# Optimization experiments

Hardware: AMD Instinct MI355X
Metric: run time of the kernel (lower is better)

The kernel has to match this reference:

```python
import jax, jax.numpy as jnp
import numpy as np

C = 256   # d_model
L = 2     # num_decoder_layers
B = 4
H = 128
W = 128
WH = 8    # dec_win_h
WW = 16   # dec_win_w
EPS = 1e-5


def _gn(x, w, b):
    # GroupNorm with 1 group: normalize over (C,H,W) per sample, per-channel affine
    mu = jnp.mean(x, axis=(1, 2, 3), keepdims=True)
    var = jnp.mean((x - mu) ** 2, axis=(1, 2, 3), keepdims=True)
    xn = (x - mu) * jax.lax.rsqrt(var + EPS)
    return xn * w[:, None, None] + b[:, None, None]


def _conv1x1(x, w, b):
    # x: [B,C,H,W], w: [O,C], b: [O]
    return jnp.einsum('bchw,oc->bohw', x, w) + b[:, None, None]


def _avgpool3(x):
    # AvgPool2d(3, stride=1, padding=1, count_include_pad=False)
    dims = (1, 1, 3, 3)
    strides = (1, 1, 1, 1)
    pad = [(0, 0), (0, 0), (1, 1), (1, 1)]
    s = jax.lax.reduce_window(x, 0.0, jax.lax.add, dims, strides, pad)
    ones = jnp.ones((1, 1) + x.shape[2:], x.dtype)
    cnt = jax.lax.reduce_window(ones, 0.0, jax.lax.add, dims, strides, pad)
    return s / cnt


def _mix(x):
    # PoolFormer token mixer: avgpool(x) - x
    return _avgpool3(x) - x


def _win_part(x, wh, ww):
    # [B,C,H,W] -> [B*nWin, C, wh, ww]
    b, c, h, w = x.shape
    x = x.reshape(b, c, h // wh, wh, w // ww, ww)
    x = x.transpose(0, 2, 4, 1, 3, 5)
    return x.reshape(-1, c, wh, ww)


def _agp(tgt, mem, qw, qb, kw, kb, vw, vb):
    # AttentionGuidedPooling; NOTE: torch uses .view(B,-1,C) on [B,C,H,W],
    # a raw reshape (not a transpose) -- replicated faithfully here.
    bw, c, h, w = mem.shape
    n = h * w
    q = _conv1x1(tgt, qw, qb).reshape(bw, n, c)
    k = _conv1x1(mem, kw, kb).reshape(bw, n, c)
    v = _conv1x1(mem, vw, vb).reshape(bw, n, c)
    attn = jax.nn.softmax(jnp.einsum('bnc,bmc->bnm', q, k), axis=-1)
    out = jnp.einsum('bnm,bmc->bnc', attn, v)
    return out.reshape(bw, c, h, w)


def _layer(tgt, mem, p):
    (gn1_w, gn1_b, gn2_w, gn2_b, ls1, ls2, ls3,
     qw, qb, kw, kb, vw, vb, fc1_w, fc1_b, fc2_w, fc2_b) = p
    tgt2 = tgt + ls1[:, None, None] * _mix(_gn(tgt, gn1_w, gn1_b))
    guided = _agp(tgt, mem, qw, qb, kw, kb, vw, vb)
    tgt3 = tgt2 + guided
    tgt3 = tgt2 + ls2[:, None, None] * _mix(_gn(tgt3, gn1_w, gn1_b))
    h = _gn(tgt3, gn2_w, gn2_b)
    h = _conv1x1(h, fc1_w, fc1_b)
    h = jax.nn.gelu(h, approximate=False)  # torch nn.GELU default (erf)
    h = _conv1x1(h, fc2_w, fc2_b)
    return tgt3 + ls3[:, None, None] * h


def setup_inputs() -> dict:
    key = jax.random.key(0)
    ks = jax.random.split(key, 16)
    s = 0.02
    inp = {
        'src': jax.random.normal(ks[0], (B, C, H, W), jnp.float32),
        'query_feats': jax.random.normal(ks[1], (B, C, H, W), jnp.float32),
        'gn1_w': jnp.ones((L, C), jnp.float32),
        'gn1_b': jnp.zeros((L, C), jnp.float32),
        'gn2_w': jnp.ones((L, C), jnp.float32),
        'gn2_b': jnp.zeros((L, C), jnp.float32),
        'ls1': 1e-5 * jnp.ones((L, C), jnp.float32),
        'ls2': 1e-5 * jnp.ones((L, C), jnp.float32),
        'ls3': 1e-5 * jnp.ones((L, C), jnp.float32),
        'qw': s * jax.random.normal(ks[2], (L, C, C), jnp.float32),
        'qb': jnp.zeros((L, C), jnp.float32),
        'kw': s * jax.random.normal(ks[3], (L, C, C), jnp.float32),
        'kb': jnp.zeros((L, C), jnp.float32),
        'vw': s * jax.random.normal(ks[4], (L, C, C), jnp.float32),
        'vb': jnp.zeros((L, C), jnp.float32),
        'fc1_w': s * jax.random.normal(ks[5], (L, 2 * C, C), jnp.float32),
        'fc1_b': jnp.zeros((L, 2 * C), jnp.float32),
        'fc2_w': s * jax.random.normal(ks[6], (L, C, 2 * C), jnp.float32),
        'fc2_b': jnp.zeros((L, C), jnp.float32),
        'gnf_w': jnp.ones((C,), jnp.float32),
        'gnf_b': jnp.zeros((C,), jnp.float32),
    }
    return inp


def reference(src, query_feats, gn1_w, gn1_b, gn2_w, gn2_b, ls1, ls2, ls3,
              qw, qb, kw, kb, vw, vb, fc1_w, fc1_b, fc2_w, fc2_b, gnf_w, gnf_b):
    # pq_stride=8 -> div_ratio=1: memory windows same size as tgt windows
    mem = _win_part(src, WH, WW)
    out = _win_part(query_feats, WH, WW)
    for l in range(L):
        p = (gn1_w[l], gn1_b[l], gn2_w[l], gn2_b[l], ls1[l], ls2[l], ls3[l],
             qw[l], qb[l], kw[l], kb[l], vw[l], vb[l],
             fc1_w[l], fc1_b[l], fc2_w[l], fc2_b[l])
        out = _layer(out, mem, p)
    out = _gn(out, gnf_w, gnf_b)
    # window reverse -> [B, C, H, W] -> sequence [B, H*W, C]
    nwh, nww = H // WH, W // WW
    x = out.reshape(B, nwh, nww, C, WH, WW).transpose(0, 3, 1, 4, 2, 5)
    x = x.reshape(B, C, H * W)
    hs = jnp.swapaxes(x, 1, 2)[None]        # [1, B, N, C]
    return jnp.swapaxes(hs, 1, 2)           # [1, N, B, C]
```

## Files before the change

kernel.cpp:

```cpp
#include <hip/hip_runtime.h>
#include <hip/hip_bf16.h>

typedef __hip_bfloat16 bf16_t;
typedef short bf16x8 __attribute__((ext_vector_type(8)));
typedef float f32x4 __attribute__((ext_vector_type(4)));

__device__ __forceinline__ float bfr(unsigned short u) {
  return __uint_as_float(((unsigned int)u) << 16);
}
__device__ __forceinline__ float b2f(bf16_t h) { return __bfloat162float(h); }
__device__ __forceinline__ bf16_t f2b(float f) { return __float2bfloat16(f); }
__device__ __forceinline__ unsigned short f2bu(float f) {
  union { bf16_t h; unsigned short u; } cv; cv.h = __float2bfloat16(f); return cv.u;
}
__device__ __forceinline__ void unpk2(unsigned int u, float& a, float& b) {
  a = __uint_as_float(u << 16);
  b = __uint_as_float(u & 0xffff0000u);
}
__device__ __forceinline__ void ld8b(const bf16_t* p, float* o) {
  uint4 v = *(const uint4*)p;
  unpk2(v.x,o[0],o[1]); unpk2(v.y,o[2],o[3]); unpk2(v.z,o[4],o[5]); unpk2(v.w,o[6],o[7]);
}
__device__ __forceinline__ void unpk8(uint4 v, float* o) {
  unpk2(v.x,o[0],o[1]); unpk2(v.y,o[2],o[3]); unpk2(v.z,o[4],o[5]); unpk2(v.w,o[6],o[7]);
}
__device__ __forceinline__ int flag_of(const void* w) {
  return (*(const unsigned int*)w == 0x3F803F80u) ? 0 : 1;
}

typedef __attribute__((address_space(3))) void lds_t;
typedef __attribute__((address_space(1))) void glb_t;
__device__ __forceinline__ void gll16(const void* g, void* l) {
  __builtin_amdgcn_global_load_lds((glb_t*)g, (lds_t*)l, 16, 0, 0);
}

struct Srcs { const void* p[18]; };

__global__ __launch_bounds__(256)
void k_cvtall(Srcs a, bf16_t* __restrict__ PR) {
  const int ck = blockIdx.x*256 + threadIdx.x;
  if (ck >= 115520) return;
  constexpr int N8[18]  = {64,64,64,64,64,64,64,64,64,128,64,32,32,16384,16384,16384,32768,32768};
  constexpr int DOF[18] = {0,512,1024,1536,2048,2560,3072,3584,4096,4608,5632,6144,6400,8192,139264,270336,401408,663552};
  int s = 0, base = 0, doff = 0, cum = 0;
#pragma unroll
  for (int i = 0; i < 17; ++i) {
    cum += N8[i];
    if (ck >= cum) { s = i + 1; base = cum; doff = DOF[i + 1]; }
  }
  const int o8 = ck - base;
  const void* sp = a.p[s];
  const int fl = flag_of(a.p[0]);
  uint4 w;
  if (fl) {
    const float4* f = (const float4*)sp;
    float4 v0 = f[o8*2], v1 = f[o8*2+1];
    w.x = ((unsigned)f2bu(v0.y)<<16) | f2bu(v0.x);
    w.y = ((unsigned)f2bu(v0.w)<<16) | f2bu(v0.z);
    w.z = ((unsigned)f2bu(v1.y)<<16) | f2bu(v1.x);
    w.w = ((unsigned)f2bu(v1.w)<<16) | f2bu(v1.z);
  } else {
    w = ((const uint4*)sp)[o8];
  }
  *(uint4*)(PR + doff + o8*8) = w;
}

__global__ __launch_bounds__(256)
void k_xt2(const void* __restrict__ inA, bf16_t* __restrict__ outA,
           const void* __restrict__ inB, bf16_t* __restrict__ outB,
           const void* __restrict__ flagw) {
  __shared__ unsigned short L[128*130];
  const void* in = blockIdx.z ? inB : inA;
  bf16_t* out = blockIdx.z ? outB : outA;
  const int win = blockIdx.x, tile = blockIdx.y, tid = threadIdx.x;
  const int IC = tile << 7;
  const int fl = flag_of(flagw);
  const int b = win >> 7, whi = (win >> 3) & 15, wwi = win & 7;

  for (int i = 0; i < 8; ++i) {
    int idx = tid + (i<<8);
    int r = idx >> 4, ch = idx & 15;
    unsigned int w0, w1, w2, w3;
    int c = IC + r;
    int hq = ch >> 1, wq = (ch & 1) << 3;
    long gaddr = ((long)((b<<8) + c) << 14) + ((whi<<3) + hq)*128 + (wwi<<4) + wq;
    if (fl) {
      const float* gp = (const float*)in + gaddr;
      float4 aa = *(const float4*)gp, bb = *(const float4*)(gp+4);
      w0 = ((unsigned)f2bu(aa.y)<<16)|f2bu(aa.x); w1 = ((unsigned)f2bu(aa.w)<<16)|f2bu(aa.z);
      w2 = ((unsigned)f2bu(bb.y)<<16)|f2bu(bb.x); w3 = ((unsigned)f2bu(bb.w)<<16)|f2bu(bb.z);
    } else {
      uint4 v = *(const uint4*)((const bf16_t*)in + gaddr);
      w0 = v.x; w1 = v.y; w2 = v.z; w3 = v.w;
    }
    unsigned int* Lp = (unsigned int*)L;
    int u32o = (r*130 + (ch<<3)) >> 1;
    Lp[u32o+0] = w0; Lp[u32o+1] = w1; Lp[u32o+2] = w2; Lp[u32o+3] = w3;
  }
  __syncthreads();
  for (int i = 0; i < 8; ++i) {
    int idx = tid + (i<<8);
    int q = idx >> 4, ch = idx & 15;
    unsigned short pk[8];
#pragma unroll
    for (int j = 0; j < 8; ++j) pk[j] = L[((ch<<3) + j)*130 + q];
    *(uint4*)(out + (long)win*32768 + (long)q*256 + IC + (ch<<3)) = *(uint4*)pk;
  }
}

__global__ __launch_bounds__(256) void k_statsP(const bf16_t* __restrict__ X, float* __restrict__ st) {
  __shared__ float s1[256], s2[256];
  int w = blockIdx.x, tid = threadIdx.x;
  const bf16_t* x = X + ((long)w << 15);
  float a = 0.f, b = 0.f;
  for (int i = tid*8; i < 32768; i += 2048) {
    float t[8]; ld8b(x + i, t);
#pragma unroll
    for (int j = 0; j < 8; ++j) { a += t[j]; b += t[j]*t[j]; }
  }
  s1[tid] = a; s2[tid] = b;
  __syncthreads();
  for (int off = 128; off > 0; off >>= 1) {
    if (tid < off) { s1[tid] += s1[tid+off]; s2[tid] += s2[tid+off]; }
    __syncthreads();
  }
  if (tid == 0) {
    float mu = s1[0] * (1.0f/32768.0f);
    float var = s2[0] * (1.0f/32768.0f) - mu*mu;
    st[(w<<1)]   = mu;
    st[(w<<1)+1] = rsqrtf(var + 1e-5f);
  }
}

template<int GATH, int GN2>
__global__ __launch_bounds__(256)
void k_poolf(const bf16_t* __restrict__ Xp, const bf16_t* __restrict__ Gc,
             bf16_t* __restrict__ Out,
             const bf16_t* __restrict__ lsv, const bf16_t* __restrict__ gw,
             bf16_t* __restrict__ G2,
             const bf16_t* __restrict__ g2w, const bf16_t* __restrict__ g2b) {
  __shared__ unsigned short L[32768];
  __shared__ float s1[256], s2[256];
  __shared__ float mr[2];
  const int win = blockIdx.x;
  const int tid = threadIdx.x;
  const long wb = (long)win << 15;
  float a = 0.f, b = 0.f;

#pragma unroll 4
  for (int i = 0; i < 16; ++i) {
    int k = (i<<8) + tid;
    int p = k >> 5, c8 = k & 31;
    uint4 v = *(const uint4*)(Xp + wb + (p<<8) + (c8<<3));
    *(uint4*)&L[(p<<8) + ((c8 ^ (p & 31))<<3)] = v;
    if (!GATH) {
      float t[8]; unpk8(v, t);
#pragma unroll
      for (int j = 0; j < 8; ++j) { a += t[j]; b += t[j]*t[j]; }
    }
  }
  if (GATH) {
    __syncthreads();
#pragma unroll 4
    for (int i = 0; i < 16; ++i) {
      int k = (i<<8) + tid;
      int c = k >> 4, p0 = (k & 15) << 3;
      uint4 gv = *(const uint4*)(Gc + wb + (c<<7) + p0);
      float g[8]; unpk8(gv, g);
      int ch = c >> 3, cl = c & 7;
#pragma unroll
      for (int j = 0; j < 8; ++j) {
        int p = p0 + j;
        int idx = (p<<8) + ((ch ^ (p & 31))<<3) + cl;
        float xx = bfr(L[idx]) + g[j];
        a += xx; b += xx*xx;
        L[idx] = f2bu(xx);
      }
    }
  }
  s1[tid] = a; s2[tid] = b;
  __syncthreads();
  for (int off = 128; off > 0; off >>= 1) {
    if (tid < off) { s1[tid] += s1[tid+off]; s2[tid] += s2[tid+off]; }
    __syncthreads();
  }
  if (tid == 0) {
    float mu = s1[0] * (1.0f/32768.0f);
    float var = s2[0] * (1.0f/32768.0f) - mu*mu;
    mr[0] = mu; mr[1] = rsqrtf(var + 1e-5f);
  }
  __syncthreads();
  const float rstd = mr[1];
  const int c = tid;
  const int ch = c >> 3, cl = c & 7;
  const float scl = b2f(lsv[c]) * b2f(gw[c]) * rstd;
  float oa = 0.f, ob = 0.f;

  float rm1[16], r0[16], rp1[16];
#pragma unroll
  for (int ww = 0; ww < 16; ++ww) {
    int p = ww;
    r0[ww] = bfr(L[(p<<8) + ((ch ^ (p & 31))<<3) + cl]);
    int p1 = 16 + ww;
    rp1[ww] = bfr(L[(p1<<8) + ((ch ^ (p1 & 31))<<3) + cl]);
  }
  for (int h = 0; h < 8; ++h) {
    float cs[16];
    float hc = 1.f + (h > 0 ? 1.f : 0.f) + (h < 7 ? 1.f : 0.f);
#pragma unroll
    for (int ww = 0; ww < 16; ++ww)
      cs[ww] = r0[ww] + (h > 0 ? rm1[ww] : 0.f) + (h < 7 ? rp1[ww] : 0.f);
#pragma unroll
    for (int ww = 0; ww < 16; ++ww) {
      float s = cs[ww];
      float wc = 1.f;
      if (ww > 0)  { s += cs[ww-1]; wc += 1.f; }
      if (ww < 15) { s += cs[ww+1]; wc += 1.f; }
      float avg = s / (hc * wc);
      float xx = r0[ww];
      int p = (h<<4) + ww;
      float base = xx;
      if (GATH) base = bfr(*(const unsigned short*)(Xp + wb + (p<<8) + c));
      float val = base + scl * (avg - xx);
      if (GN2) {
        oa += val; ob += val*val;
        L[(p<<8) + ((ch ^ (p & 31))<<3) + cl] = f2bu(val);
      }
      Out[wb + (p<<8) + c] = f2b(val);
    }
#pragma unroll
    for (int ww = 0; ww < 16; ++ww) { rm1[ww] = r0[ww]; r0[ww] = rp1[ww]; }
    if (h < 6) {
      int hp = (h+2) << 4;
#pragma unroll
      for (int ww = 0; ww < 16; ++ww) {
        int p = hp + ww;
        rp1[ww] = bfr(L[(p<<8) + ((ch ^ (p & 31))<<3) + cl]);
      }
    }
  }
  if (GN2) {
    __syncthreads();
    s1[tid] = oa; s2[tid] = ob;
    __syncthreads();
    for (int off = 128; off > 0; off >>= 1) {
      if (tid < off) { s1[tid] += s1[tid+off]; s2[tid] += s2[tid+off]; }
      __syncthreads();
    }
    if (tid == 0) {
      float mu = s1[0] * (1.0f/32768.0f);
      float var = s2[0] * (1.0f/32768.0f) - mu*mu;
      mr[0] = mu; mr[1] = rsqrtf(var + 1e-5f);
    }
    __syncthreads();
    const float mu2 = mr[0], rs2 = mr[1];
#pragma unroll 4
    for (int i = 0; i < 16; ++i) {
      int k = (i<<8) + tid;
      int p = k >> 5, cv = k & 31;
      uint4 v = *(const uint4*)&L[(p<<8) + ((cv ^ (p & 31))<<3)];
      float t[8]; unpk8(v, t);
      uint4 wv = *(const uint4*)(g2w + (cv<<3));
      uint4 bv = *(const uint4*)(g2b + (cv<<3));
      float wf[8], bf2[8]; unpk8(wv, wf); unpk8(bv, bf2);
      unsigned short pk[8];
#pragma unroll
      for (int j = 0; j < 8; ++j) pk[j] = f2bu((t[j]-mu2)*rs2*wf[j] + bf2[j]);
      *(uint4*)(G2 + wb + (p<<8) + (cv<<3)) = *(uint4*)pk;
    }
  }
}

#define GM_QKV  0
#define GM_NM   1
#define GM_GELU 2
#define GM_RES  3

template<int MODE>
__global__ __launch_bounds__(256, 2)
void k_gemm(const bf16_t* __restrict__ A, long sA, int lda,
            const bf16_t* __restrict__ B0, const bf16_t* __restrict__ B1,
            long sB, int ldb,
            bf16_t* __restrict__ Y, long sY, int ldy,
            const bf16_t* __restrict__ bias,
            const bf16_t* __restrict__ res, long sR,
            const bf16_t* __restrict__ ls,
            int K) {
  __shared__ uint4 LB[2048];
  unsigned short* As = (unsigned short*)LB;
  unsigned short* Bs = (unsigned short*)LB + 8192;
  unsigned short* E  = (unsigned short*)LB;
  const int win = blockIdx.x;
  const int tid = threadIdx.x;
  const int w = tid >> 6, lane = tid & 63;
  const int l15 = lane & 15, quad = lane >> 4;
  const int m0w = (w >> 1) << 6, n0w = (w & 1) << 6;

  int sel = 0, m0;
  const bf16_t *Ab, *Bb; bf16_t* Yb; const bf16_t* biasb = nullptr;
  if (MODE == GM_QKV) {
    sel = blockIdx.y >> 1; m0 = (blockIdx.y & 1) << 7;
    Ab = A + sel*131072 + (long)m0*lda;
    Bb = (sel ? B1 : B0) + (long)win*sB;
    Yb = Y + (long)sel*16777216 + (long)win*sY;
    biasb = bias + sel*512 + m0;
  } else {
    m0 = blockIdx.y << 7;
    Ab = A + (long)win*sA + (long)m0*lda;
    Bb = B0 + (long)win*sB;
    Yb = Y + (long)win*sY;
    if (bias) biasb = bias + m0;
  }
  const bool CT = (MODE == GM_QKV) && (sel < 2);

  int rr_[4], co_[4], lo_[4];
#pragma unroll
  for (int j = 0; j < 4; ++j) {
    int ck = (j<<8) + (w<<6) + lane;
    int r = ck >> 3;
    rr_[j] = r;
    co_[j] = ((ck & 7) ^ (r & 7)) << 3;
    lo_[j] = ((j<<8) + (w<<6)) << 3;
  }

  f32x4 acc[4][4];
#pragma unroll
  for (int i = 0; i < 4; ++i)
#pragma unroll
    for (int j = 0; j < 4; ++j) acc[i][j] = (f32x4){0.f,0.f,0.f,0.f};

  for (int k0 = 0; k0 < K; k0 += 64) {
#pragma unroll
    for (int j = 0; j < 4; ++j) {
      gll16(Ab + (long)rr_[j]*lda + k0 + co_[j], As + lo_[j]);
      gll16(Bb + (long)rr_[j]*ldb + k0 + co_[j], Bs + lo_[j]);
    }
    __syncthreads();
#pragma unroll
    for (int kk = 0; kk < 2; ++kk) {
      bf16x8 af[4], bv[4];
#pragma unroll
      for (int im = 0; im < 4; ++im) {
        int R = m0w + (im<<4) + l15;
        af[im] = *(const bf16x8*)&As[(R<<6) + ((((kk<<2)+quad) ^ (R&7))<<3)];
      }
#pragma unroll
      for (int in = 0; in < 4; ++in) {
        int R = n0w + (in<<4) + l15;
        bv[in] = *(const bf16x8*)&Bs[(R<<6) + ((((kk<<2)+quad) ^ (R&7))<<3)];
      }
      if (CT) {
#pragma unroll
        for (int im = 0; im < 4; ++im)
#pragma unroll
          for (int in = 0; in < 4; ++in)
            acc[im][in] = __builtin_amdgcn_mfma_f32_16x16x32_bf16(bv[in], af[im], acc[im][in], 0, 0, 0);
      } else {
#pragma unroll
        for (int im = 0; im < 4; ++im)
#pragma unroll
          for (int in = 0; in < 4; ++in)
            acc[im][in] = __builtin_amdgcn_mfma_f32_16x16x32_bf16(af[im], bv[in], acc[im][in], 0, 0, 0);
      }
    }
    __syncthreads();
  }

  if (MODE == GM_QKV && sel == 2) {
#pragma unroll
    for (int im = 0; im < 4; ++im) {
#pragma unroll
      for (int in = 0; in < 4; ++in) {
        f32x4 v = acc[im][in];
        int tok = n0w + (in<<4) + l15;
        int c0 = m0w + (im<<4) + (quad<<2);
        int u0 = c0 >> 1;
        float x0 = v[0] + b2f(biasb[c0]);
        float x1 = v[1] + b2f(biasb[c0+1]);
        float x2 = v[2] + b2f(biasb[c0+2]);
        float x3 = v[3] + b2f(biasb[c0+3]);
        int sl = (((u0>>3) ^ (tok&7))<<3) + (u0&7);
        *(unsigned int*)&E[(tok<<6) + sl]       = (unsigned)f2bu(x0) | ((unsigned)f2bu(x2)<<16);
        *(unsigned int*)&E[((128+tok)<<6) + sl] = (unsigned)f2bu(x1) | ((unsigned)f2bu(x3)<<16);
      }
    }
    __syncthreads();
#pragma unroll
    for (int i = 0; i < 8; ++i) {
      int ck = (i<<8) + tid;
      int cp = ck >> 3, u8 = ck & 7;
      uint4 v = *(const uint4*)&E[(cp<<6) + ((u8 ^ (cp&7))<<3)];
      *(uint4*)(Yb + (long)cp*128 + (m0>>1) + (u8<<3)) = v;
    }
    return;
  }

  if (CT) {
#pragma unroll
    for (int half = 0; half < 2; ++half) {
      if (m0w == (half<<6)) {
#pragma unroll
        for (int im = 0; im < 4; ++im) {
          int row = (im<<4) + l15;
          float bm = b2f(biasb[(half<<6) + row]);
#pragma unroll
          for (int in = 0; in < 4; ++in) {
            f32x4 v = acc[im][in];
            unsigned short pk[4];
#pragma unroll
            for (int r = 0; r < 4; ++r) pk[r] = f2bu(v[r] + bm);
            *(ushort4*)&E[row*136 + n0w + (in<<4) + (quad<<2)] = *(ushort4*)pk;
          }
        }
      }
      __syncthreads();
#pragma unroll
      for (int i = 0; i < 4; ++i) {
        int ck = (i<<8) + tid;
        int row = ck >> 4, c8 = (ck & 15) << 3;
        uint4 v = *(const uint4*)&E[row*136 + c8];
        *(uint4*)(Yb + (long)(m0 + (half<<6) + row)*ldy + c8) = v;
      }
      __syncthreads();
    }
    return;
  }

#pragma unroll
  for (int half = 0; half < 2; ++half) {
    if (n0w == (half<<6)) {
#pragma unroll
      for (int in = 0; in < 4; ++in) {
        int row = (in<<4) + l15;
#pragma unroll
        for (int im = 0; im < 4; ++im) {
          f32x4 v = acc[im][in];
          int mb = m0w + (im<<4) + (quad<<2);
          unsigned short pk[4];
#pragma unroll
          for (int r = 0; r < 4; ++r) {
            float x = v[r];
            if (MODE == GM_GELU || MODE == GM_RES) x += b2f(biasb[mb + r]);
            if (MODE == GM_GELU) x = 0.5f * x * (1.0f + erff(x * 0.70710678118654752f));
            pk[r] = f2bu(x);
          }
          *(ushort4*)&E[row*136 + mb] = *(ushort4*)pk;
        }
      }
    }
    __syncthreads();
#pragma unroll
    for (int i = 0; i < 4; ++i) {
      int ck = (i<<8) + tid;
      int rloc = ck >> 4, c8 = (ck & 15) << 3;
      long oadr = (long)((half<<6) + rloc)*ldy + m0 + c8;
      uint4 v = *(const uint4*)&E[rloc*136 + c8];
      if (MODE == GM_RES) {
        float t[8]; unpk8(v, t);
        uint4 rv = *(const uint4*)(res + (long)win*sR + oadr);
        float rf[8]; unpk8(rv, rf);
        uint4 lv = *(const uint4*)(ls + m0 + c8);
        float lf[8]; unpk8(lv, lf);
        unsigned short pk[8];
#pragma unroll
        for (int j = 0; j < 8; ++j) pk[j] = f2bu(rf[j] + lf[j]*t[j]);
        *(uint4*)(Yb + oadr) = *(uint4*)pk;
      } else {
        *(uint4*)(Yb + oadr) = v;
      }
    }
    __syncthreads();
  }
}

__global__ __launch_bounds__(256, 2)
void k_scores(const bf16_t* __restrict__ Kc, const bf16_t* __restrict__ Qc,
              bf16_t* __restrict__ P) {
  __shared__ uint4 LB[2048];
  __shared__ float red[2][2][128];
  unsigned short* As = (unsigned short*)LB;
  unsigned short* Bs = (unsigned short*)LB + 8192;
  const int win = blockIdx.x;
  const int tid = threadIdx.x;
  const int w = tid >> 6, lane = tid & 63;
  const int l15 = lane & 15, quad = lane >> 4;
  const int m0w = (w >> 1) << 6, n0w = (w & 1) << 6;
  const int wrow = w >> 1;
  const bf16_t* Ab = Kc + ((long)win << 15);
  const bf16_t* Bb = Qc + ((long)win << 15);

  int rr_[4], co_[4], lo_[4];
#pragma unroll
  for (int j = 0; j < 4; ++j) {
    int ck = (j<<8) + (w<<6) + lane;
    int r = ck >> 3;
    rr_[j] = r;
    co_[j] = ((ck & 7) ^ (r & 7)) << 3;
    lo_[j] = ((j<<8) + (w<<6)) << 3;
  }

  f32x4 acc[4][4];
#pragma unroll
  for (int i = 0; i < 4; ++i)
#pragma unroll
    for (int j = 0; j < 4; ++j) acc[i][j] = (f32x4){0.f,0.f,0.f,0.f};

  for (int k0 = 0; k0 < 256; k0 += 64) {
#pragma unroll
    for (int j = 0; j < 4; ++j) {
      gll16(Ab + (long)rr_[j]*256 + k0 + co_[j], As + lo_[j]);
      gll16(Bb + (long)rr_[j]*256 + k0 + co_[j], Bs + lo_[j]);
    }
    __syncthreads();
#pragma unroll
    for (int kk = 0; kk < 2; ++kk) {
      bf16x8 af[4], bv[4];
#pragma unroll
      for (int im = 0; im < 4; ++im) {
        int R = m0w + (im<<4) + l15;
        af[im] = *(const bf16x8*)&As[(R<<6) + ((((kk<<2)+quad) ^ (R&7))<<3)];
      }
#pragma unroll
      for (int in = 0; in < 4; ++in) {
        int R = n0w + (in<<4) + l15;
        bv[in] = *(const bf16x8*)&Bs[(R<<6) + ((((kk<<2)+quad) ^ (R&7))<<3)];
      }
#pragma unroll
      for (int im = 0; im < 4; ++im)
#pragma unroll
        for (int in = 0; in < 4; ++in)
          acc[im][in] = __builtin_amdgcn_mfma_f32_16x16x32_bf16(af[im], bv[in], acc[im][in], 0, 0, 0);
    }
    __syncthreads();
  }

  float mx[4];
#pragma unroll
  for (int in = 0; in < 4; ++in) {
    float m = -3.4e38f;
#pragma unroll
    for (int im = 0; im < 4; ++im)
#pragma unroll
      for (int r = 0; r < 4; ++r) m = fmaxf(m, acc[im][in][r]);
    m = fmaxf(m, __shfl_xor(m, 16));
    m = fmaxf(m, __shfl_xor(m, 32));
    mx[in] = m;
  }
  if (quad == 0) {
#pragma unroll
    for (int in = 0; in < 4; ++in) red[0][wrow][n0w + (in<<4) + l15] = mx[in];
  }
  __syncthreads();
  float fm[4];
#pragma unroll
  for (int in = 0; in < 4; ++in) {
    int t = n0w + (in<<4) + l15;
    fm[in] = fmaxf(red[0][0][t], red[0][1][t]);
  }
  float sm[4];
#pragma unroll
  for (int in = 0; in < 4; ++in) {
    float s = 0.f;
#pragma unroll
    for (int im = 0; im < 4; ++im)
#pragma unroll
      for (int r = 0; r < 4; ++r) {
        float e = __expf(acc[im][in][r] - fm[in]);
        acc[im][in][r] = e;
        s += e;
      }
    s += __shfl_xor(s, 16);
    s += __shfl_xor(s, 32);
    sm[in] = s;
  }
  if (quad == 0) {
#pragma unroll
    for (int in = 0; in < 4; ++in) red[1][wrow][n0w + (in<<4) + l15] = sm[in];
  }
  __syncthreads();
  bf16_t* Pw = P + ((long)win << 14);
#pragma unroll
  for (int in = 0; in < 4; ++in) {
    int t = n0w + (in<<4) + l15;
    float inv = 1.0f / (red[1][0][t] + red[1][1][t]);
#pragma unroll
    for (int im = 0; im < 4; ++im) {
      int u = m0w + (im<<4) + (quad<<2);
      unsigned short pk[4];
#pragma unroll
      for (int r = 0; r < 4; ++r) pk[r] = f2bu(acc[im][in][r] * inv);
      *(ushort4*)(Pw + t*128 + u) = *(ushort4*)pk;
    }
  }
}

__global__ void k_final(const bf16_t* __restrict__ Tp, const float* __restrict__ st,
                        const bf16_t* __restrict__ gw, const bf16_t* __restrict__ gb,
                        void* __restrict__ out, const void* __restrict__ flagw) {
  const int fl = flag_of(flagw);
  int idx = blockIdx.x*256 + threadIdx.x;
  int c = idx & 255, p = (idx >> 8) & 127, win = idx >> 15;
  float mu = st[win*2], rs = st[win*2+1];
  float v = (b2f(Tp[idx]) - mu) * rs * b2f(gw[c]) + b2f(gb[c]);
  int b = win >> 7, whi = (win >> 3) & 15, wwi = win & 7;
  int n = ((whi<<3) + (p>>4)) * 128 + (wwi<<4) + (p & 15);
  long o = ((long)((n<<2) + b) << 8) + c;
  if (fl) ((float*)out)[o] = v;
  else    ((bf16_t*)out)[o] = f2b(v);
}

extern "C" void kernel_launch(void* const* d_in, const int* in_sizes, int n_in,
                              void* d_out, int out_size, void* d_ws, size_t ws_size,
                              hipStream_t stream) {
  (void)in_sizes; (void)n_in; (void)out_size; (void)ws_size;
  const void* src   = d_in[0];
  const void* qfeat = d_in[1];

  bf16_t* W    = (bf16_t*)d_ws;
  bf16_t* Tp   = W;
  bf16_t* T2p  = W + 16777216;
  bf16_t* Sp   = W + 33554432;
  bf16_t* slA  = W + 50331648;
  bf16_t* KcGc = W + 67108864;
  bf16_t* Vc   = W + 83886080;
  bf16_t* Hp   = KcGc;
  bf16_t* P    = W + 100663296;
  bf16_t* PR   = W + 109051904;
  float*  ST   = (float*)(W + 110100480);
  float*  st0  = ST;

  bf16_t* gn1w = PR;
  bf16_t* gn2w = PR + 512;
  bf16_t* gn2b = PR + 1024;
  bf16_t* ls1  = PR + 1536;
  bf16_t* ls2  = PR + 2048;
  bf16_t* ls3  = PR + 2560;
  bf16_t* qb   = PR + 3072;
  bf16_t* f1b  = PR + 4608;
  bf16_t* f2bp = PR + 5632;
  bf16_t* gfw  = PR + 6144;
  bf16_t* gfb  = PR + 6400;
  bf16_t* qw   = PR + 8192;
  bf16_t* f1w  = PR + 401408;
  bf16_t* f2w  = PR + 663552;

  Srcs sa;
  const int map[18] = {2,4,5,6,7,8,10,12,14,16,18,19,20,9,11,13,15,17};
  for (int i = 0; i < 18; ++i) sa.p[i] = d_in[map[i]];
  k_cvtall<<<452, 256, 0, stream>>>(sa, PR);

  k_xt2<<<dim3(512,2,2), 256, 0, stream>>>(qfeat, Tp, src, Sp, d_in[2]);

  for (int l = 0; l < 2; ++l) {
    k_poolf<0,0><<<512, 256, 0, stream>>>(Tp, nullptr, T2p, ls1 + l*256, gn1w + l*256,
                                          nullptr, nullptr, nullptr);
    k_gemm<GM_QKV><<<dim3(512,6), 256, 0, stream>>>(
        qw + l*65536, 0, 256, Tp, Sp, 32768, 256, slA, 32768, 128,
        qb + l*256, nullptr, 0, nullptr, 256);
    k_scores<<<512, 256, 0, stream>>>(KcGc, slA, P);
    k_gemm<GM_NM><<<dim3(512,2), 256, 0, stream>>>(
        Vc, 32768, 128, P, nullptr, 16384, 128, KcGc, 32768, 256,
        nullptr, nullptr, 0, nullptr, 128);
    k_poolf<1,1><<<512, 256, 0, stream>>>(T2p, KcGc, Tp, ls2 + l*256, gn1w + l*256,
                                          slA, gn2w + l*256, gn2b + l*256);
    k_gemm<GM_GELU><<<dim3(512,4), 256, 0, stream>>>(
        f1w + l*131072, 0, 256, slA, nullptr, 32768, 256, Hp, 65536, 512,
        f1b + l*512, nullptr, 0, nullptr, 256);
    k_gemm<GM_RES><<<dim3(512,2), 256, 0, stream>>>(
        f2w + l*131072, 0, 512, Hp, nullptr, 65536, 512, Tp, 32768, 256,
        f2bp + l*256, Tp, 32768, ls3 + l*256, 512);
  }

  k_statsP<<<512, 256, 0, stream>>>(Tp, st0);
  k_final<<<65536, 256, 0, stream>>>(Tp, st0, gfw, gfb, d_out, d_in[2]);
}
```

Before: 817.0 us.

## Split poolformer rows across 512 threads, use shuffle reductions, vectorize final GroupNorm

k_poolf now runs 512 threads per window. Each half of the block handles four of the eight window rows, and the LDS swizzle is changed to match. Block reductions use wavefront xor-shuffles plus an 8-entry shared array instead of a 256-step tree with many barriers. The GN2 pass re-reads its values from the global output rather than rewriting them into LDS, since the two halves would otherwise race. The final normalize/scatter kernel now processes 8 channels per thread with vector loads and stores, replacing one element per thread, which cuts its launch to an eighth as many blocks.

```diff
diff --git a/kernel.cpp b/kernel.cpp
--- a/kernel.cpp
+++ b/kernel.cpp
@@ -133,26 +133,26 @@
 }
 
 template<int GATH, int GN2>
-__global__ __launch_bounds__(256)
+__global__ __launch_bounds__(512, 4)
 void k_poolf(const bf16_t* __restrict__ Xp, const bf16_t* __restrict__ Gc,
              bf16_t* __restrict__ Out,
              const bf16_t* __restrict__ lsv, const bf16_t* __restrict__ gw,
              bf16_t* __restrict__ G2,
              const bf16_t* __restrict__ g2w, const bf16_t* __restrict__ g2b) {
   __shared__ unsigned short L[32768];
-  __shared__ float s1[256], s2[256];
+  __shared__ float s1[8], s2[8];
   __shared__ float mr[2];
   const int win = blockIdx.x;
   const int tid = threadIdx.x;
   const long wb = (long)win << 15;
   float a = 0.f, b = 0.f;
 
-#pragma unroll 4
-  for (int i = 0; i < 16; ++i) {
-    int k = (i<<8) + tid;
+#pragma unroll
+  for (int i = 0; i < 8; ++i) {
+    int k = (i<<9) + tid;
     int p = k >> 5, c8 = k & 31;
     uint4 v = *(const uint4*)(Xp + wb + (p<<8) + (c8<<3));
-    *(uint4*)&L[(p<<8) + ((c8 ^ (p & 31))<<3)] = v;
+    *(uint4*)&L[(p<<8) + ((c8 ^ ((p>>3)&7))<<3)] = v;
     if (!GATH) {
       float t[8]; unpk8(v, t);
 #pragma unroll
@@ -161,37 +161,39 @@
   }
   if (GATH) {
     __syncthreads();
-#pragma unroll 4
-    for (int i = 0; i < 16; ++i) {
-      int k = (i<<8) + tid;
+#pragma unroll
+    for (int i = 0; i < 8; ++i) {
+      int k = (i<<9) + tid;
       int c = k >> 4, p0 = (k & 15) << 3;
       uint4 gv = *(const uint4*)(Gc + wb + (c<<7) + p0);
       float g[8]; unpk8(gv, g);
       int ch = c >> 3, cl = c & 7;
+      int sl = ((ch ^ ((p0>>3) & 7))<<3) + cl;
 #pragma unroll
       for (int j = 0; j < 8; ++j) {
-        int p = p0 + j;
-        int idx = (p<<8) + ((ch ^ (p & 31))<<3) + cl;
+        int idx = ((p0 + j)<<8) + sl;
         float xx = bfr(L[idx]) + g[j];
         a += xx; b += xx*xx;
         L[idx] = f2bu(xx);
       }
     }
   }
-  s1[tid] = a; s2[tid] = b;
+#pragma unroll
+  for (int d = 1; d < 64; d <<= 1) { a += __shfl_xor(a, d); b += __shfl_xor(b, d); }
+  if ((tid & 63) == 0) { s1[tid>>6] = a; s2[tid>>6] = b; }
   __syncthreads();
-  for (int off = 128; off > 0; off >>= 1) {
-    if (tid < off) { s1[tid] += s1[tid+off]; s2[tid] += s2[tid+off]; }
-    __syncthreads();
-  }
   if (tid == 0) {
-    float mu = s1[0] * (1.0f/32768.0f);
-    float var = s2[0] * (1.0f/32768.0f) - mu*mu;
+    float sa = 0.f, sb = 0.f;
+#pragma unroll
+    for (int i = 0; i < 8; ++i) { sa += s1[i]; sb += s2[i]; }
+    float mu = sa * (1.0f/32768.0f);
+    float var = sb * (1.0f/32768.0f) - mu*mu;
     mr[0] = mu; mr[1] = rsqrtf(var + 1e-5f);
   }
   __syncthreads();
   const float rstd = mr[1];
-  const int c = tid;
+  const int c = tid & 255;
+  const int hb = (tid >> 8) << 2;
   const int ch = c >> 3, cl = c & 7;
   const float scl = b2f(lsv[c]) * b2f(gw[c]) * rstd;
   float oa = 0.f, ob = 0.f;
@@ -199,12 +201,21 @@
   float rm1[16], r0[16], rp1[16];
 #pragma unroll
   for (int ww = 0; ww < 16; ++ww) {
-    int p = ww;
-    r0[ww] = bfr(L[(p<<8) + ((ch ^ (p & 31))<<3) + cl]);
-    int p1 = 16 + ww;
-    rp1[ww] = bfr(L[(p1<<8) + ((ch ^ (p1 & 31))<<3) + cl]);
-  }
-  for (int h = 0; h < 8; ++h) {
+    int p0_ = (hb<<4) + ww;
+    r0[ww] = bfr(L[(p0_<<8) + ((ch ^ ((p0_>>3)&7))<<3) + cl]);
+    int p1_ = ((hb+1)<<4) + ww;
+    rp1[ww] = bfr(L[(p1_<<8) + ((ch ^ ((p1_>>3)&7))<<3) + cl]);
+  }
+  if (hb > 0) {
+#pragma unroll
+    for (int ww = 0; ww < 16; ++ww) {
+      int pm = ((hb-1)<<4) + ww;
+      rm1[ww] = bfr(L[(pm<<8) + ((ch ^ ((pm>>3)&7))<<3) + cl]);
+    }
+  }
+#pragma unroll
+  for (int hl = 0; hl < 4; ++hl) {
+    int h = hb + hl;
     float cs[16];
     float hc = 1.f + (h > 0 ? 1.f : 0.f) + (h < 7 ? 1.f : 0.f);
 #pragma unroll
@@ -222,43 +233,40 @@
       float base = xx;
       if (GATH) base = bfr(*(const unsigned short*)(Xp + wb + (p<<8) + c));
       float val = base + scl * (avg - xx);
-      if (GN2) {
-        oa += val; ob += val*val;
-        L[(p<<8) + ((ch ^ (p & 31))<<3) + cl] = f2bu(val);
-      }
+      if (GN2) { oa += val; ob += val*val; }
       Out[wb + (p<<8) + c] = f2b(val);
     }
 #pragma unroll
     for (int ww = 0; ww < 16; ++ww) { rm1[ww] = r0[ww]; r0[ww] = rp1[ww]; }
-    if (h < 6) {
+    if (hl < 3 && (h + 2) <= 7) {
       int hp = (h+2) << 4;
 #pragma unroll
       for (int ww = 0; ww < 16; ++ww) {
         int p = hp + ww;
-        rp1[ww] = bfr(L[(p<<8) + ((ch ^ (p & 31))<<3) + cl]);
+        rp1[ww] = bfr(L[(p<<8) + ((ch ^ ((p>>3)&7))<<3) + cl]);
       }
     }
   }
   if (GN2) {
-    __syncthreads();
-    s1[tid] = oa; s2[tid] = ob;
-    __syncthreads();
-    for (int off = 128; off > 0; off >>= 1) {
-      if (tid < off) { s1[tid] += s1[tid+off]; s2[tid] += s2[tid+off]; }
-      __syncthreads();
-    }
+#pragma unroll
+    for (int d = 1; d < 64; d <<= 1) { oa += __shfl_xor(oa, d); ob += __shfl_xor(ob, d); }
+    if ((tid & 63) == 0) { s1[tid>>6] = oa; s2[tid>>6] = ob; }
+    __syncthreads();
     if (tid == 0) {
-      float mu = s1[0] * (1.0f/32768.0f);
-      float var = s2[0] * (1.0f/32768.0f) - mu*mu;
+      float sa = 0.f, sb = 0.f;
+#pragma unroll
+      for (int i = 0; i < 8; ++i) { sa += s1[i]; sb += s2[i]; }
+      float mu = sa * (1.0f/32768.0f);
+      float var = sb * (1.0f/32768.0f) - mu*mu;
       mr[0] = mu; mr[1] = rsqrtf(var + 1e-5f);
     }
     __syncthreads();
     const float mu2 = mr[0], rs2 = mr[1];
-#pragma unroll 4
-    for (int i = 0; i < 16; ++i) {
-      int k = (i<<8) + tid;
+#pragma unroll
+    for (int i = 0; i < 8; ++i) {
+      int k = (i<<9) + tid;
       int p = k >> 5, cv = k & 31;
-      uint4 v = *(const uint4*)&L[(p<<8) + ((cv ^ (p & 31))<<3)];
+      uint4 v = *(const uint4*)(Out + wb + (p<<8) + (cv<<3));
       float t[8]; unpk8(v, t);
       uint4 wv = *(const uint4*)(g2w + (cv<<3));
       uint4 bv = *(const uint4*)(g2b + (cv<<3));
@@ -594,19 +602,37 @@
   }
 }
 
-__global__ void k_final(const bf16_t* __restrict__ Tp, const float* __restrict__ st,
-                        const bf16_t* __restrict__ gw, const bf16_t* __restrict__ gb,
-                        void* __restrict__ out, const void* __restrict__ flagw) {
+__global__ __launch_bounds__(256)
+void k_final(const bf16_t* __restrict__ Tp, const float* __restrict__ st,
+             const bf16_t* __restrict__ gw, const bf16_t* __restrict__ gb,
+             void* __restrict__ out, const void* __restrict__ flagw) {
   const int fl = flag_of(flagw);
-  int idx = blockIdx.x*256 + threadIdx.x;
-  int c = idx & 255, p = (idx >> 8) & 127, win = idx >> 15;
+  long k = (long)blockIdx.x*256 + threadIdx.x;
+  int c8 = (int)(k & 31), p = (int)((k >> 5) & 127), win = (int)(k >> 12);
   float mu = st[win*2], rs = st[win*2+1];
-  float v = (b2f(Tp[idx]) - mu) * rs * b2f(gw[c]) + b2f(gb[c]);
+  uint4 v = *(const uint4*)(Tp + (k<<3));
+  float t[8]; unpk8(v, t);
+  uint4 wv = *(const uint4*)(gw + (c8<<3));
+  uint4 bv = *(const uint4*)(gb + (c8<<3));
+  float wf[8], bf2[8]; unpk8(wv, wf); unpk8(bv, bf2);
+  float o_[8];
+#pragma unroll
+  for (int j = 0; j < 8; ++j) o_[j] = (t[j] - mu) * rs * wf[j] + bf2[j];
   int b = win >> 7, whi = (win >> 3) & 15, wwi = win & 7;
   int n = ((whi<<3) + (p>>4)) * 128 + (wwi<<4) + (p & 15);
-  long o = ((long)((n<<2) + b) << 8) + c;
-  if (fl) ((float*)out)[o] = v;
-  else    ((bf16_t*)out)[o] = f2b(v);
+  long o = ((long)((n<<2) + b) << 8) + (c8<<3);
+  if (fl) {
+    float4 f0, f1;
+    f0.x=o_[0]; f0.y=o_[1]; f0.z=o_[2]; f0.w=o_[3];
+    f1.x=o_[4]; f1.y=o_[5]; f1.z=o_[6]; f1.w=o_[7];
+    *(float4*)((float*)out + o)     = f0;
+    *(float4*)((float*)out + o + 4) = f1;
+  } else {
+    unsigned short pk[8];
+#pragma unroll
+    for (int j = 0; j < 8; ++j) pk[j] = f2bu(o_[j]);
+    *(uint4*)((bf16_t*)out + o) = *(uint4*)pk;
+  }
 }
 
 extern "C" void kernel_launch(void* const* d_in, const int* in_sizes, int n_in,
@@ -652,7 +678,7 @@
   k_xt2<<<dim3(512,2,2), 256, 0, stream>>>(qfeat, Tp, src, Sp, d_in[2]);
 
   for (int l = 0; l < 2; ++l) {
-    k_poolf<0,0><<<512, 256, 0, stream>>>(Tp, nullptr, T2p, ls1 + l*256, gn1w + l*256,
+    k_poolf<0,0><<<512, 512, 0, stream>>>(Tp, nullptr, T2p, ls1 + l*256, gn1w + l*256,
                                           nullptr, nullptr, nullptr);
     k_gemm<GM_QKV><<<dim3(512,6), 256, 0, stream>>>(
         qw + l*65536, 0, 256, Tp, Sp, 32768, 256, slA, 32768, 128,
@@ -661,7 +687,7 @@
     k_gemm<GM_NM><<<dim3(512,2), 256, 0, stream>>>(
         Vc, 32768, 128, P, nullptr, 16384, 128, KcGc, 32768, 256,
         nullptr, nullptr, 0, nullptr, 128);
-    k_poolf<1,1><<<512, 256, 0, stream>>>(T2p, KcGc, Tp, ls2 + l*256, gn1w + l*256,
+    k_poolf<1,1><<<512, 512, 0, stream>>>(T2p, KcGc, Tp, ls2 + l*256, gn1w + l*256,
                                           slA, gn2w + l*256, gn2b + l*256);
     k_gemm<GM_GELU><<<dim3(512,4), 256, 0, stream>>>(
         f1w + l*131072, 0, 256, slA, nullptr, 32768, 256, Hp, 65536, 512,
@@ -672,5 +698,5 @@
   }
 
   k_statsP<<<512, 256, 0, stream>>>(Tp, st0);
-  k_final<<<65536, 256, 0, stream>>>(Tp, st0, gfw, gfb, d_out, d_in[2]);
-}
+  k_final<<<8192, 256, 0, stream>>>(Tp, st0, gfw, gfb, d_out, d_in[2]);
+}
```

Result: faster. 739.7 us (-9.5%).
